# Kernel tuning notes

Hardware: AMD Instinct MI355X
Metric: run time of the kernel (lower is better)

## Reference

```python
import jax, jax.numpy as jnp
import numpy as np
import itertools

# config: dim=256, resolution=14, key_dim=32, heads=8, attention_ratio=4, act=gelu (exact)
B, DIM, RES = 128, 256, 14
H, KD, DV = 8, 32, 128          # heads, key_dim, int(attention_ratio*key_dim)
N = RES * RES                    # 196 tokens
DH = H * DV                      # dim_head = 1024
SCALE = KD ** -0.5


def _bias_idxs():
    points = list(itertools.product(range(RES), range(RES)))
    offsets, idxs = {}, []
    for p1 in points:
        for p2 in points:
            off = (abs(p1[0] - p2[0]), abs(p1[1] - p2[1]))
            if off not in offsets:
                offsets[off] = len(offsets)
            idxs.append(offsets[off])
    return np.asarray(idxs, np.int32).reshape(N, N), len(offsets)


def _cbn(x, w, b, s, t):
    # 1x1 conv (as channel GEMM) + inference BatchNorm folded to per-channel affine
    y = jnp.einsum('bchw,co->bohw', x, w) + b[None, :, None, None]
    return y * s[None, :, None, None] + t[None, :, None, None]


def setup_inputs() -> dict:
    key = jax.random.key(0)
    ks = jax.random.split(key, 32)
    n = lambda i, sh, sc=0.05: jax.random.normal(ks[i], sh, jnp.float32) * sc
    idxs, noff = _bias_idxs()
    return {
        'hidden_states': jax.random.normal(ks[0], (B, DIM, RES, RES), jnp.float32),
        'w_q': n(1, (DIM, H * KD)), 'b_q': n(2, (H * KD,)), 's_q': 1.0 + n(3, (H * KD,)), 't_q': n(4, (H * KD,)),
        'w_k': n(5, (DIM, H * KD)), 'b_k': n(6, (H * KD,)), 's_k': 1.0 + n(7, (H * KD,)), 't_k': n(8, (H * KD,)),
        'w_v': n(9, (DIM, DH)), 'b_v': n(10, (DH,)), 's_v': 1.0 + n(11, (DH,)), 't_v': n(12, (DH,)),
        'w_vl': n(13, (DH, 1, 3, 3)), 'b_vl': n(14, (DH,)), 's_vl': 1.0 + n(15, (DH,)), 't_vl': n(16, (DH,)),
        'w_th1': n(17, (H, H), 0.2), 'b_th1': n(18, (H,)),
        'w_th2': n(19, (H, H), 0.2), 'b_th2': n(20, (H,)),
        'w_p': n(21, (DH, DIM)), 'b_p': n(22, (DIM,)), 's_p': 1.0 + n(23, (DIM,)), 't_p': n(24, (DIM,)),
        'attention_biases': n(25, (H, noff), 0.2),
        'bias_idxs': jnp.asarray(idxs),
    }


def reference(hidden_states, w_q, b_q, s_q, t_q, w_k, b_k, s_k, t_k,
              w_v, b_v, s_v, t_v, w_vl, b_vl, s_vl, t_vl,
              w_th1, b_th1, w_th2, b_th2, w_p, b_p, s_p, t_p,
              attention_biases, bias_idxs):
    b = hidden_states.shape[0]
    q = _cbn(hidden_states, w_q, b_q, s_q, t_q).reshape(b, H, KD, N).transpose(0, 1, 3, 2)  # [B,H,N,kd]
    k = _cbn(hidden_states, w_k, b_k, s_k, t_k).reshape(b, H, KD, N)                        # [B,H,kd,N]
    v_img = _cbn(hidden_states, w_v, b_v, s_v, t_v)                                          # [B,DH,res,res]
    vl = jax.lax.conv_general_dilated(v_img, w_vl, (1, 1), ((1, 1), (1, 1)),
                                      feature_group_count=DH,
                                      dimension_numbers=('NCHW', 'OIHW', 'NCHW'))
    vl = (vl + b_vl[None, :, None, None]) * s_vl[None, :, None, None] + t_vl[None, :, None, None]
    v = v_img.reshape(b, H, DV, N).transpose(0, 1, 3, 2)                                     # [B,H,N,dv]

    ab = attention_biases[:, bias_idxs]                                                      # [H,N,N]
    attn = jnp.einsum('bhnk,bhkm->bhnm', q, k) * SCALE + ab[None]                            # [B,H,N,N]
    attn = jnp.einsum('gh,bhnm->bgnm', w_th1, attn) + b_th1[None, :, None, None]             # talking head 1
    attn = jax.nn.softmax(attn, axis=-1)
    attn = jnp.einsum('gh,bhnm->bgnm', w_th2, attn) + b_th2[None, :, None, None]             # talking head 2

    out = jnp.einsum('bhnm,bhmd->bhnd', attn, v)                                             # [B,H,N,dv]
    out = out.transpose(0, 1, 3, 2).reshape(b, DH, RES, RES) + vl
    out = jax.nn.gelu(out, approximate=False)                                                # torch GELU (exact)
    return _cbn(out, w_p, b_p, s_p, t_p)                                                     # [B,dim,res,res]
```

## Files before the change

### kernel.cpp

```cpp
#include <hip/hip_runtime.h>
#include <hip/hip_bf16.h>

typedef __hip_bfloat16 bf16;
typedef __attribute__((ext_vector_type(8))) short bf16x8;
typedef __attribute__((ext_vector_type(8))) unsigned short u16x8;
typedef __attribute__((ext_vector_type(4))) float f32x4;

#define NB 128
#define CIN 256
#define NPIX 196
#define RESW 14
#define NH 8
#define KD 32
#define DV 128
#define DHID 1024
#define QKSCALE 0.17677669529663687f
#define QT 16
#define NTILE 13
#define VSTRIDE 224
#define ZPAD 232
#define XSP 264
#define GROWS 208

__device__ __forceinline__ float bf2f(unsigned short u) {
  union { unsigned int i; float f; } x; x.i = ((unsigned int)u) << 16; return x.f;
}
__device__ __forceinline__ unsigned short f2bfs(float f) {
  union { float f; unsigned int i; } u; u.f = f;
  unsigned int r = u.i + 0x7fffu + ((u.i >> 16) & 1u);
  return (unsigned short)(r >> 16);
}
__device__ __forceinline__ float gelu_exact(float x) {
  return x * 0.5f * (1.f + erff(x * 0.70710678118654752f));
}

__global__ void k_fold(
    const float* wq, const float* bq, const float* sq, const float* tq,
    const float* wk, const float* bk, const float* sk, const float* tk,
    const float* wv, const float* bv, const float* sv, const float* tv,
    const float* wvl, const float* bvl_in, const float* svl, const float* tvl,
    const float* wp, const float* bp_in, const float* sp, const float* tp,
    const float* abias, const int* bidx, const float* w1, const float* b1,
    int noff,
    short* Wt, short* Wpt, float* bcat, float* bpf, float* Wvl, float* bvlf,
    float* AB1)
{
  int i = blockIdx.x * 256 + threadIdx.x;
  if (i < 393216) {
    int o = i >> 8, c = i & 255;
    float w, s;
    if (o < 256)      { w = wq[c * 256 + o];          s = sq[o]; }
    else if (o < 512) { w = wk[c * 256 + (o - 256)];  s = sk[o - 256]; }
    else              { w = wv[c * 1024 + (o - 512)]; s = sv[o - 512]; }
    Wt[i] = (short)f2bfs(w * s);
    return;
  }
  i -= 393216;
  if (i < 1536) {
    float b, s, t;
    if (i < 256)      { b = bq[i];        s = sq[i];        t = tq[i]; }
    else if (i < 512) { b = bk[i - 256];  s = sk[i - 256];  t = tk[i - 256]; }
    else              { b = bv[i - 512];  s = sv[i - 512];  t = tv[i - 512]; }
    bcat[i] = b * s + t;
    return;
  }
  i -= 1536;
  if (i < 262144) {
    int o = i >> 10, ch = i & 1023;
    Wpt[i] = (short)f2bfs(wp[ch * 256 + o] * sp[o]);
    return;
  }
  i -= 262144;
  if (i < 256) { bpf[i] = bp_in[i] * sp[i] + tp[i]; return; }
  i -= 256;
  if (i < 9216) { int ch = i / 9; Wvl[i] = wvl[i] * svl[ch]; return; }
  i -= 9216;
  if (i < 1024) { bvlf[i] = bvl_in[i] * svl[i] + tvl[i]; return; }
  i -= 1024;
  if (i < NPIX * NPIX) {
    int idx = bidx[i];
    float a[8];
#pragma unroll
    for (int h = 0; h < 8; ++h) a[h] = abias[h * noff + idx];
#pragma unroll
    for (int g = 0; g < 8; ++g) {
      float z = b1[g];
#pragma unroll
      for (int h = 0; h < 8; ++h) z += w1[g * 8 + h] * a[h];
      AB1[(size_t)g * NPIX * NPIX + i] = z;
    }
    return;
  }
}

__global__ __launch_bounds__(512) void k_qkv(
    const float* __restrict__ X, const short* __restrict__ Wt,
    const float* __restrict__ bcat, bf16* __restrict__ Yq,
    bf16* __restrict__ Yk, bf16* __restrict__ Yv)
{
  __shared__ short Xs[64 * XSP];
  int b = blockIdx.x >> 2, q = blockIdx.x & 3;
  const int qs_[4] = {0, 4, 7, 10};
  const int qc_[4] = {4, 3, 3, 3};
  int qs = qs_[q], qc = qc_[q];
  int rowbase = qs * 16, nrows = qc * 16;
  int t = threadIdx.x;
  const float* Xb = X + (size_t)b * CIN * NPIX;

  int jn = nrows >> 2;
  for (int i = t; i < 256 * jn; i += 512) {
    int c = i / jn, j = i % jn;
    int ng = rowbase + 4 * j;
    int lr = 4 * j;
    if (ng + 3 < NPIX) {
      float4 xv = *(const float4*)(Xb + c * NPIX + ng);
      Xs[(lr + 0) * XSP + c] = (short)f2bfs(xv.x);
      Xs[(lr + 1) * XSP + c] = (short)f2bfs(xv.y);
      Xs[(lr + 2) * XSP + c] = (short)f2bfs(xv.z);
      Xs[(lr + 3) * XSP + c] = (short)f2bfs(xv.w);
    } else {
#pragma unroll
      for (int e = 0; e < 4; ++e) {
        float v = (ng + e < NPIX) ? Xb[c * NPIX + ng + e] : 0.f;
        Xs[(lr + e) * XSP + c] = (short)f2bfs(v);
      }
    }
  }
  __syncthreads();

  int w = t >> 6, lane = t & 63, nl = lane & 15, grp = lane >> 4;

  for (int mm = w; mm < 96; mm += 8) {
    if (mm < 32) {
      int ot = mm;
      const short* arow = Wt + (size_t)(ot * 16 + nl) * CIN;
      f32x4 acc[4];
#pragma unroll
      for (int s = 0; s < 4; ++s) acc[s] = (f32x4){0.f, 0.f, 0.f, 0.f};
#pragma unroll
      for (int kk = 0; kk < 8; ++kk) {
        bf16x8 af = *(const bf16x8*)(arow + kk * 32 + grp * 8);
#pragma unroll
        for (int s = 0; s < 4; ++s) {
          if (s < qc) {
            bf16x8 bfr = *(const bf16x8*)(Xs + (s * 16 + nl) * XSP + kk * 32 + grp * 8);
            acc[s] = __builtin_amdgcn_mfma_f32_16x16x32_bf16(af, bfr, acc[s], 0, 0, 0);
          }
        }
      }
      int o0 = ot * 16 + grp * 4;
      float4 bb = *(const float4*)(bcat + o0);
      unsigned short* dst = (unsigned short*)((o0 < 256) ? Yq : Yk);
      int ob = o0 & 255;
#pragma unroll
      for (int s = 0; s < 4; ++s) {
        if (s < qc) {
          int n = (qs + s) * 16 + nl;
          if (n < NPIX) {
            ushort4 pk;
            pk.x = f2bfs(acc[s][0] + bb.x); pk.y = f2bfs(acc[s][1] + bb.y);
            pk.z = f2bfs(acc[s][2] + bb.z); pk.w = f2bfs(acc[s][3] + bb.w);
            *(ushort4*)(dst + ((size_t)b * NPIX + n) * CIN + ob) = pk;
          }
        }
      }
    } else {
      int cht = mm - 32;
      int ch = cht * 16 + nl;
      const short* brow = Wt + (size_t)(512 + ch) * CIN;
      f32x4 acc[4];
#pragma unroll
      for (int s = 0; s < 4; ++s) acc[s] = (f32x4){0.f, 0.f, 0.f, 0.f};
#pragma unroll
      for (int kk = 0; kk < 8; ++kk) {
        bf16x8 bfr = *(const bf16x8*)(brow + kk * 32 + grp * 8);
#pragma unroll
        for (int s = 0; s < 4; ++s) {
          if (s < qc) {
            bf16x8 af = *(const bf16x8*)(Xs + (s * 16 + nl) * XSP + kk * 32 + grp * 8);
            acc[s] = __builtin_amdgcn_mfma_f32_16x16x32_bf16(af, bfr, acc[s], 0, 0, 0);
          }
        }
      }
      float bb = bcat[512 + ch];
#pragma unroll
      for (int s = 0; s < 4; ++s) {
        if (s < qc) {
          int m0 = (qs + s) * 16 + grp * 4;
          if (m0 + 3 < NPIX) {
            ushort4 pk;
            pk.x = f2bfs(acc[s][0] + bb); pk.y = f2bfs(acc[s][1] + bb);
            pk.z = f2bfs(acc[s][2] + bb); pk.w = f2bfs(acc[s][3] + bb);
            *(ushort4*)((unsigned short*)Yv + ((size_t)b * DHID + ch) * VSTRIDE + m0) = pk;
          }
        }
      }
    }
  }
}

__global__ __launch_bounds__(512) void k_conv(
    const bf16* __restrict__ Yv, const float* __restrict__ Wvl,
    const float* __restrict__ bvlf, bf16* __restrict__ Gt)
{
  __shared__ short Vs[128 * ZPAD];
  int b = blockIdx.x >> 3, cg = blockIdx.x & 7;
  int t = threadIdx.x;
  const unsigned short* src = (const unsigned short*)Yv + ((size_t)b * DHID + cg * 128) * VSTRIDE;
  for (int i = t; i < 128 * 28; i += 512) {
    int ch = i / 28, j = i % 28;
    u16x8 v = *(const u16x8*)(src + ch * VSTRIDE + j * 8);
    *(u16x8*)(Vs + ch * ZPAD + j * 8) = v;
  }
  __syncthreads();

  int ch = t & 127, yg = t >> 7;
  int chg = cg * 128 + ch;
  float w9[9];
#pragma unroll
  for (int k = 0; k < 9; ++k) w9[k] = Wvl[chg * 9 + k];
  float bb = bvlf[chg];
  const short* row = Vs + ch * ZPAD;
  unsigned short* gbase = (unsigned short*)Gt + (size_t)b * GROWS * DHID + chg;

  int ylim = (yg == 3) ? 2 : 4;
  for (int yy = 0; yy < ylim; ++yy) {
    int y = yg * 4 + yy;
    float rw[3][14];
#pragma unroll
    for (int dy = 0; dy < 3; ++dy) {
      int ys = y + dy - 1;
      if (ys < 0 || ys >= RESW) {
#pragma unroll
        for (int x = 0; x < 14; ++x) rw[dy][x] = 0.f;
      } else {
#pragma unroll
        for (int x2 = 0; x2 < 7; ++x2) {
          unsigned int u = *(const unsigned int*)(row + ys * RESW + x2 * 2);
          rw[dy][x2 * 2]     = bf2f((unsigned short)(u & 0xffffu));
          rw[dy][x2 * 2 + 1] = bf2f((unsigned short)(u >> 16));
        }
      }
    }
#pragma unroll
    for (int x = 0; x < 14; ++x) {
      float a = bb;
#pragma unroll
      for (int dy = 0; dy < 3; ++dy)
#pragma unroll
        for (int dx = 0; dx < 3; ++dx) {
          int xx = x + dx - 1;
          if (xx >= 0 && xx < RESW) a += w9[dy * 3 + dx] * rw[dy][xx];
        }
      gbase[(size_t)(y * RESW + x) * DHID] = f2bfs(a);
    }
  }
}

__global__ __launch_bounds__(512, 4) void k_attn(
    const bf16* __restrict__ Yq, const bf16* __restrict__ Yk,
    const bf16* __restrict__ Yv, const float* __restrict__ AB1,
    const float* __restrict__ w1, const float* __restrict__ w2,
    const float* __restrict__ b2, bf16* __restrict__ Gt)
{
  __shared__ short zb[NH][QT][ZPAD];
  __shared__ float red[8][NH][16];
  int id = blockIdx.x;
  int swz = (id & 7) * (NB * NTILE / 8) + (id >> 3);
  int b = swz / NTILE, tile = swz % NTILE;
  int n0 = tile * QT;
  int t = threadIdx.x;
  int w = t >> 6, lane = t & 63;
  int nl = lane & 15, grp = lane >> 4;
  int n = n0 + nl;
  int nA = (n < NPIX) ? n : (NPIX - 1);

  int t0 = w;
  int t1 = (w < 5) ? (w + 8) : ((w == 5) ? 13 : -1);

  const short* qrow = (const short*)Yq + ((size_t)b * NPIX + nA) * CIN;
  bf16x8 qf[8];
#pragma unroll
  for (int h = 0; h < 8; ++h) qf[h] = *(const bf16x8*)(qrow + h * 32 + grp * 8);

  const short* kbase = (const short*)Yk + (size_t)b * NPIX * CIN;
  const f32x4 NEG = (f32x4){-1e30f, -1e30f, -1e30f, -1e30f};
  f32x4 zm0[8], zm1[8];

#define DO_TILE(MT, ZM)                                                        \
  {                                                                            \
    int m0_ = (MT) * 16 + grp * 4;                                             \
    bool mv_ = ((MT) < 13) && (m0_ + 3 < NPIX);                                \
    _Pragma("unroll")                                                          \
    for (int g = 0; g < 8; ++g) {                                              \
      ZM[g] = mv_ ? (*(const f32x4*)(AB1 + ((size_t)g * NPIX + nA) * NPIX + m0_)) \
                  : NEG;                                                       \
    }                                                                          \
    if ((MT) < 13) {                                                           \
      int mrow_ = (MT) * 16 + nl; if (mrow_ > NPIX - 1) mrow_ = NPIX - 1;      \
      const short* krow_ = kbase + (size_t)mrow_ * CIN + grp * 8;              \
      _Pragma("unroll")                                                        \
      for (int h = 0; h < 8; ++h) {                                            \
        bf16x8 kf_ = *(const bf16x8*)(krow_ + h * 32);                         \
        f32x4 zr_ = __builtin_amdgcn_mfma_f32_16x16x32_bf16(                   \
            kf_, qf[h], (f32x4){0.f, 0.f, 0.f, 0.f}, 0, 0, 0);                 \
        _Pragma("unroll")                                                      \
        for (int g = 0; g < 8; ++g) {                                          \
          float wgh_ = w1[g * 8 + h] * QKSCALE;                                \
          _Pragma("unroll")                                                    \
          for (int r = 0; r < 4; ++r) ZM[g][r] += wgh_ * zr_[r];               \
        }                                                                      \
      }                                                                        \
    }                                                                          \
  }

  DO_TILE(t0, zm0)
  if (t1 >= 0) { DO_TILE(t1, zm1) }
  else {
#pragma unroll
    for (int g = 0; g < 8; ++g) zm1[g] = NEG;
  }

  float mg[8];
#pragma unroll
  for (int g = 0; g < 8; ++g) {
    float m_ = fmaxf(fmaxf(zm0[g][0], zm0[g][1]), fmaxf(zm0[g][2], zm0[g][3]));
    m_ = fmaxf(m_, fmaxf(fmaxf(zm1[g][0], zm1[g][1]), fmaxf(zm1[g][2], zm1[g][3])));
    m_ = fmaxf(m_, __shfl_xor(m_, 16));
    m_ = fmaxf(m_, __shfl_xor(m_, 32));
    mg[g] = m_;
  }
  if (lane < 16) {
#pragma unroll
    for (int g = 0; g < 8; ++g) red[w][g][nl] = mg[g];
  }
  __syncthreads();
  float fmx[8];
#pragma unroll
  for (int g = 0; g < 8; ++g) {
    float m_ = red[0][g][nl];
#pragma unroll
    for (int ww = 1; ww < 8; ++ww) m_ = fmaxf(m_, red[ww][g][nl]);
    fmx[g] = m_;
  }
  float sg[8];
#pragma unroll
  for (int g = 0; g < 8; ++g) {
    float s_ = 0.f;
#pragma unroll
    for (int r = 0; r < 4; ++r) { zm0[g][r] = __expf(zm0[g][r] - fmx[g]); s_ += zm0[g][r]; }
#pragma unroll
    for (int r = 0; r < 4; ++r) { zm1[g][r] = __expf(zm1[g][r] - fmx[g]); s_ += zm1[g][r]; }
    s_ += __shfl_xor(s_, 16);
    s_ += __shfl_xor(s_, 32);
    sg[g] = s_;
  }
  __syncthreads();
  if (lane < 16) {
#pragma unroll
    for (int g = 0; g < 8; ++g) red[w][g][nl] = sg[g];
  }
  __syncthreads();
  float inv[8];
#pragma unroll
  for (int g = 0; g < 8; ++g) {
    float s_ = red[0][g][nl];
#pragma unroll
    for (int ww = 1; ww < 8; ++ww) s_ += red[ww][g][nl];
    inv[g] = 1.f / s_;
  }

#define MIX_WR(MT, ZM)                                                         \
  {                                                                            \
    int m0_ = (MT) * 16 + grp * 4;                                             \
    bool v_ = (m0_ + 3 < NPIX);                                                \
    float aj_[8][4];                                                           \
    _Pragma("unroll")                                                          \
    for (int j = 0; j < 8; ++j) {                                              \
      float bj_ = b2[j];                                                       \
      _Pragma("unroll")                                                        \
      for (int r = 0; r < 4; ++r) aj_[j][r] = bj_;                             \
    }                                                                          \
    _Pragma("unroll")                                                          \
    for (int g = 0; g < 8; ++g) {                                              \
      float pr_[4];                                                            \
      _Pragma("unroll")                                                        \
      for (int r = 0; r < 4; ++r) pr_[r] = ZM[g][r] * inv[g];                  \
      _Pragma("unroll")                                                        \
      for (int j = 0; j < 8; ++j) {                                            \
        float wj_ = w2[j * 8 + g];                                             \
        _Pragma("unroll")                                                      \
        for (int r = 0; r < 4; ++r) aj_[j][r] += wj_ * pr_[r];                 \
      }                                                                        \
    }                                                                          \
    _Pragma("unroll")                                                          \
    for (int j = 0; j < 8; ++j) {                                              \
      ushort4 pk_;                                                             \
      if (v_) { pk_.x = f2bfs(aj_[j][0]); pk_.y = f2bfs(aj_[j][1]);            \
                pk_.z = f2bfs(aj_[j][2]); pk_.w = f2bfs(aj_[j][3]); }          \
      else    { pk_.x = 0; pk_.y = 0; pk_.z = 0; pk_.w = 0; }                  \
      *(ushort4*)&zb[j][nl][m0_] = pk_;                                        \
    }                                                                          \
  }
  MIX_WR(t0, zm0)
  if (t1 >= 0) { MIX_WR(t1, zm1) }

  unsigned short* gp = (unsigned short*)Gt + ((size_t)b * GROWS + nA) * DHID + w * DV;
  ushort4 cvv[8];
#pragma unroll
  for (int dt = 0; dt < 8; ++dt) cvv[dt] = *(const ushort4*)(gp + dt * 16 + grp * 4);
  __syncthreads();

  f32x4 accO[8];
#pragma unroll
  for (int dt = 0; dt < 8; ++dt) accO[dt] = (f32x4){0.f, 0.f, 0.f, 0.f};
  const short* vbase = (const short*)Yv + ((size_t)b * DHID + w * DV) * VSTRIDE;
#pragma unroll
  for (int ks = 0; ks < 7; ++ks) {
    int moff = ks * 32 + grp * 8;
    bf16x8 Bf = *(const bf16x8*)&zb[w][nl][moff];
#pragma unroll
    for (int dt = 0; dt < 8; ++dt) {
      bf16x8 Af = *(const bf16x8*)(vbase + (size_t)(dt * 16 + nl) * VSTRIDE + moff);
      accO[dt] = __builtin_amdgcn_mfma_f32_16x16x32_bf16(Af, Bf, accO[dt], 0, 0, 0);
    }
  }

  if (n < NPIX) {
#pragma unroll
    for (int dt = 0; dt < 8; ++dt) {
      ushort4 pk;
      float pre;
      pre = accO[dt][0] + bf2f(cvv[dt].x); pk.x = f2bfs(gelu_exact(pre));
      pre = accO[dt][1] + bf2f(cvv[dt].y); pk.y = f2bfs(gelu_exact(pre));
      pre = accO[dt][2] + bf2f(cvv[dt].z); pk.z = f2bfs(gelu_exact(pre));
      pre = accO[dt][3] + bf2f(cvv[dt].w); pk.w = f2bfs(gelu_exact(pre));
      *(ushort4*)(gp + dt * 16 + grp * 4) = pk;
    }
  }
}

__global__ __launch_bounds__(512) void k_proj(
    const bf16* __restrict__ Gt, const short* __restrict__ Wpt,
    const float* __restrict__ bpf, float* __restrict__ out)
{
  int b = blockIdx.x >> 1, nhalf = blockIdx.x & 1;
  int t = threadIdx.x, w = t >> 6, lane = t & 63, nl = lane & 15, grp = lane >> 4;
  int ot0 = w, ot1 = w + 8;
  int ntb = nhalf * 7;
  int NTH = nhalf ? 6 : 7;
  const short* a0 = Wpt + (size_t)(ot0 * 16 + nl) * DHID + grp * 8;
  const short* a1 = Wpt + (size_t)(ot1 * 16 + nl) * DHID + grp * 8;
  const short* bb = (const short*)Gt + (size_t)b * GROWS * DHID
                  + (size_t)(ntb * 16 + nl) * DHID + grp * 8;
  f32x4 acc0[7], acc1[7];
#pragma unroll
  for (int i = 0; i < 7; ++i) {
    acc0[i] = (f32x4){0.f, 0.f, 0.f, 0.f};
    acc1[i] = (f32x4){0.f, 0.f, 0.f, 0.f};
  }
  for (int kk = 0; kk < 32; ++kk) {
    bf16x8 af0 = *(const bf16x8*)(a0 + kk * 32);
    bf16x8 af1 = *(const bf16x8*)(a1 + kk * 32);
#pragma unroll
    for (int nt = 0; nt < 7; ++nt) {
      if (nt < NTH) {
        bf16x8 bfr = *(const bf16x8*)(bb + (size_t)(nt * 16) * DHID + kk * 32);
        acc0[nt] = __builtin_amdgcn_mfma_f32_16x16x32_bf16(af0, bfr, acc0[nt], 0, 0, 0);
        acc1[nt] = __builtin_amdgcn_mfma_f32_16x16x32_bf16(af1, bfr, acc1[nt], 0, 0, 0);
      }
    }
  }
  int o0 = ot0 * 16 + grp * 4;
  int o1 = ot1 * 16 + grp * 4;
  float4 b0 = *(const float4*)(bpf + o0);
  float4 b1v = *(const float4*)(bpf + o1);
  float b0a[4] = {b0.x, b0.y, b0.z, b0.w};
  float b1a[4] = {b1v.x, b1v.y, b1v.z, b1v.w};
#pragma unroll
  for (int nt = 0; nt < 7; ++nt) {
    if (nt < NTH) {
      int nn = (ntb + nt) * 16 + nl;
      if (nn < NPIX) {
#pragma unroll
        for (int r = 0; r < 4; ++r) {
          out[((size_t)b * CIN + o0 + r) * NPIX + nn] = acc0[nt][r] + b0a[r];
          out[((size_t)b * CIN + o1 + r) * NPIX + nn] = acc1[nt][r] + b1a[r];
        }
      }
    }
  }
}

extern "C" void kernel_launch(void* const* d_in, const int* in_sizes, int n_in,
                              void* d_out, int out_size, void* d_ws, size_t ws_size,
                              hipStream_t stream) {
  const float* X    = (const float*)d_in[0];
  const float* wq   = (const float*)d_in[1];
  const float* bq   = (const float*)d_in[2];
  const float* sq   = (const float*)d_in[3];
  const float* tq   = (const float*)d_in[4];
  const float* wk   = (const float*)d_in[5];
  const float* bk   = (const float*)d_in[6];
  const float* sk   = (const float*)d_in[7];
  const float* tk   = (const float*)d_in[8];
  const float* wv   = (const float*)d_in[9];
  const float* bv   = (const float*)d_in[10];
  const float* sv   = (const float*)d_in[11];
  const float* tv   = (const float*)d_in[12];
  const float* wvl  = (const float*)d_in[13];
  const float* bvl  = (const float*)d_in[14];
  const float* svl  = (const float*)d_in[15];
  const float* tvl  = (const float*)d_in[16];
  const float* w1   = (const float*)d_in[17];
  const float* b1   = (const float*)d_in[18];
  const float* w2   = (const float*)d_in[19];
  const float* b2   = (const float*)d_in[20];
  const float* wp   = (const float*)d_in[21];
  const float* bpp  = (const float*)d_in[22];
  const float* sp   = (const float*)d_in[23];
  const float* tp   = (const float*)d_in[24];
  const float* ab   = (const float*)d_in[25];
  const int*   bidx = (const int*)d_in[26];
  int noff = in_sizes[25] / NH;

  short* Wt   = (short*)d_ws;
  short* Wpt  = Wt + 393216;
  float* bcat = (float*)(Wpt + 262144);
  float* bpf  = bcat + 1536;
  float* Wvl  = bpf + 256;
  float* bvlf = Wvl + 9216;
  float* AB1  = bvlf + 1024;
  short* Yq   = (short*)(AB1 + 307328);
  short* Yk   = Yq + (size_t)NB * NPIX * CIN;
  short* Yv   = Yk + (size_t)NB * NPIX * CIN;
  short* Gt   = Yv + (size_t)NB * DHID * VSTRIDE;

  k_fold<<<2758, 256, 0, stream>>>(wq, bq, sq, tq, wk, bk, sk, tk,
                                   wv, bv, sv, tv, wvl, bvl, svl, tvl,
                                   wp, bpp, sp, tp, ab, bidx, w1, b1, noff,
                                   Wt, Wpt, bcat, bpf, Wvl, bvlf, AB1);
  k_qkv<<<NB * 4, 512, 0, stream>>>(X, Wt, bcat, (bf16*)Yq, (bf16*)Yk, (bf16*)Yv);
  k_conv<<<NB * 8, 512, 0, stream>>>((const bf16*)Yv, Wvl, bvlf, (bf16*)Gt);
  k_attn<<<NB * NTILE, 512, 0, stream>>>((const bf16*)Yq, (const bf16*)Yk,
                                         (const bf16*)Yv, AB1, w1, w2, b2, (bf16*)Gt);
  k_proj<<<NB * 2, 512, 0, stream>>>((const bf16*)Gt, Wpt, bpf, (float*)d_out);
}
```

Before: 489.5 us.

## Recompute attention scores in two passes to cut register pressure

Instead of holding both score tiles (zm0, zm1) in registers across the softmax, the kernel now computes scores once to find the row max, then recomputes them to take exponentials. It stores the unnormalized exponentials as bf16 in shared memory and reads them back for the talking-head mix. This is meant to lower VGPR usage, and so spills or occupancy limits, at the cost of a second QK MFMA pass plus bias reload. The extra bf16 rounding of the exponentials before normalization adds some precision loss.

```diff
diff --git a/kernel.cpp b/kernel.cpp
--- a/kernel.cpp
+++ b/kernel.cpp
@@ -285,17 +285,15 @@
 
   const short* kbase = (const short*)Yk + (size_t)b * NPIX * CIN;
   const f32x4 NEG = (f32x4){-1e30f, -1e30f, -1e30f, -1e30f};
-  f32x4 zm0[8], zm1[8];
-
-#define DO_TILE(MT, ZM)                                                        \
+
+#define SCORES(MT, ZM)                                                         \
   {                                                                            \
     int m0_ = (MT) * 16 + grp * 4;                                             \
     bool mv_ = ((MT) < 13) && (m0_ + 3 < NPIX);                                \
     _Pragma("unroll")                                                          \
-    for (int g = 0; g < 8; ++g) {                                              \
+    for (int g = 0; g < 8; ++g)                                                \
       ZM[g] = mv_ ? (*(const f32x4*)(AB1 + ((size_t)g * NPIX + nA) * NPIX + m0_)) \
                   : NEG;                                                       \
-    }                                                                          \
     if ((MT) < 13) {                                                           \
       int mrow_ = (MT) * 16 + nl; if (mrow_ > NPIX - 1) mrow_ = NPIX - 1;      \
       const short* krow_ = kbase + (size_t)mrow_ * CIN + grp * 8;              \
@@ -314,21 +312,26 @@
     }                                                                          \
   }
 
-  DO_TILE(t0, zm0)
-  if (t1 >= 0) { DO_TILE(t1, zm1) }
-  else {
-#pragma unroll
-    for (int g = 0; g < 8; ++g) zm1[g] = NEG;
-  }
-
   float mg[8];
 #pragma unroll
+  for (int g = 0; g < 8; ++g) mg[g] = -1e30f;
+  {
+    f32x4 zt[8];
+    SCORES(t0, zt)
+#pragma unroll
+    for (int g = 0; g < 8; ++g)
+      mg[g] = fmaxf(mg[g], fmaxf(fmaxf(zt[g][0], zt[g][1]), fmaxf(zt[g][2], zt[g][3])));
+    if (t1 >= 0) {
+      SCORES(t1, zt)
+#pragma unroll
+      for (int g = 0; g < 8; ++g)
+        mg[g] = fmaxf(mg[g], fmaxf(fmaxf(zt[g][0], zt[g][1]), fmaxf(zt[g][2], zt[g][3])));
+    }
+  }
+#pragma unroll
   for (int g = 0; g < 8; ++g) {
-    float m_ = fmaxf(fmaxf(zm0[g][0], zm0[g][1]), fmaxf(zm0[g][2], zm0[g][3]));
-    m_ = fmaxf(m_, fmaxf(fmaxf(zm1[g][0], zm1[g][1]), fmaxf(zm1[g][2], zm1[g][3])));
-    m_ = fmaxf(m_, __shfl_xor(m_, 16));
-    m_ = fmaxf(m_, __shfl_xor(m_, 32));
-    mg[g] = m_;
+    mg[g] = fmaxf(mg[g], __shfl_xor(mg[g], 16));
+    mg[g] = fmaxf(mg[g], __shfl_xor(mg[g], 32));
   }
   if (lane < 16) {
 #pragma unroll
@@ -343,19 +346,41 @@
     for (int ww = 1; ww < 8; ++ww) m_ = fmaxf(m_, red[ww][g][nl]);
     fmx[g] = m_;
   }
+  __syncthreads();
+
   float sg[8];
 #pragma unroll
+  for (int g = 0; g < 8; ++g) sg[g] = 0.f;
+#define EXPWR(MT, ZM)                                                          \
+  {                                                                            \
+    int m0_ = (MT) * 16 + grp * 4;                                             \
+    _Pragma("unroll")                                                          \
+    for (int g = 0; g < 8; ++g) {                                              \
+      float e0_ = __expf(ZM[g][0] - fmx[g]);                                   \
+      float e1_ = __expf(ZM[g][1] - fmx[g]);                                   \
+      float e2_ = __expf(ZM[g][2] - fmx[g]);                                   \
+      float e3_ = __expf(ZM[g][3] - fmx[g]);                                   \
+      sg[g] += (e0_ + e1_) + (e2_ + e3_);                                      \
+      ushort4 pk_;                                                             \
+      pk_.x = f2bfs(e0_); pk_.y = f2bfs(e1_);                                  \
+      pk_.z = f2bfs(e2_); pk_.w = f2bfs(e3_);                                  \
+      *(ushort4*)&zb[g][nl][m0_] = pk_;                                        \
+    }                                                                          \
+  }
+  {
+    f32x4 zt[8];
+    SCORES(t0, zt)
+    EXPWR(t0, zt)
+    if (t1 >= 0) {
+      SCORES(t1, zt)
+      EXPWR(t1, zt)
+    }
+  }
+#pragma unroll
   for (int g = 0; g < 8; ++g) {
-    float s_ = 0.f;
-#pragma unroll
-    for (int r = 0; r < 4; ++r) { zm0[g][r] = __expf(zm0[g][r] - fmx[g]); s_ += zm0[g][r]; }
-#pragma unroll
-    for (int r = 0; r < 4; ++r) { zm1[g][r] = __expf(zm1[g][r] - fmx[g]); s_ += zm1[g][r]; }
-    s_ += __shfl_xor(s_, 16);
-    s_ += __shfl_xor(s_, 32);
-    sg[g] = s_;
-  }
-  __syncthreads();
+    sg[g] += __shfl_xor(sg[g], 16);
+    sg[g] += __shfl_xor(sg[g], 32);
+  }
   if (lane < 16) {
 #pragma unroll
     for (int g = 0; g < 8; ++g) red[w][g][nl] = sg[g];
@@ -370,10 +395,10 @@
     inv[g] = 1.f / s_;
   }
 
-#define MIX_WR(MT, ZM)                                                         \
+#define MIX3(MT)                                                               \
   {                                                                            \
     int m0_ = (MT) * 16 + grp * 4;                                             \
-    bool v_ = (m0_ + 3 < NPIX);                                                \
+    bool v_ = (m0_ + 3 < NPIX) && ((MT) < 13);                                 \
     float aj_[8][4];                                                           \
     _Pragma("unroll")                                                          \
     for (int j = 0; j < 8; ++j) {                                              \
@@ -383,14 +408,16 @@
     }                                                                          \
     _Pragma("unroll")                                                          \
     for (int g = 0; g < 8; ++g) {                                              \
-      float pr_[4];                                                            \
-      _Pragma("unroll")                                                        \
-      for (int r = 0; r < 4; ++r) pr_[r] = ZM[g][r] * inv[g];                  \
+      ushort4 e_ = *(const ushort4*)&zb[g][nl][m0_];                           \
+      float p0_ = bf2f(e_.x) * inv[g];                                         \
+      float p1_ = bf2f(e_.y) * inv[g];                                         \
+      float p2_ = bf2f(e_.z) * inv[g];                                         \
+      float p3_ = bf2f(e_.w) * inv[g];                                         \
       _Pragma("unroll")                                                        \
       for (int j = 0; j < 8; ++j) {                                            \
         float wj_ = w2[j * 8 + g];                                             \
-        _Pragma("unroll")                                                      \
-        for (int r = 0; r < 4; ++r) aj_[j][r] += wj_ * pr_[r];                 \
+        aj_[j][0] += wj_ * p0_; aj_[j][1] += wj_ * p1_;                        \
+        aj_[j][2] += wj_ * p2_; aj_[j][3] += wj_ * p3_;                        \
       }                                                                        \
     }                                                                          \
     _Pragma("unroll")                                                          \
@@ -402,8 +429,8 @@
       *(ushort4*)&zb[j][nl][m0_] = pk_;                                        \
     }                                                                          \
   }
-  MIX_WR(t0, zm0)
-  if (t1 >= 0) { MIX_WR(t1, zm1) }
+  MIX3(t0)
+  if (t1 >= 0) { MIX3(t1) }
 
   unsigned short* gp = (unsigned short*)Gt + ((size_t)b * GROWS + nA) * DHID + w * DV;
   ushort4 cvv[8];
```

After: 499.1 us. About the same (+2.0%).
